# Performance work log

Hardware: AMD Instinct MI355X
Metric: run time of the kernel (lower is better)

## Reference

```python
import jax, jax.numpy as jnp
import numpy as np

N = 100000   # nodes
E = 1600000  # edges
IN_DIM = 256
HID = 128
OUT_DIM = 64
LAYERS = 3
LN_EPS = 1e-5


def _layer_norm(y, g, b):
    mu = jnp.mean(y, axis=-1, keepdims=True)
    var = jnp.mean(jnp.square(y - mu), axis=-1, keepdims=True)
    return (y - mu) * jax.lax.rsqrt(var + LN_EPS) * g + b


def _gcn_conv(x, W, b, src, dst, norm):
    # x: [N, H]; W: [H, H]; src/dst: [E+N] (self-loops appended); norm: [E+N]
    xw = x @ W
    msg = xw[src] * norm[:, None]                       # [E+N, H] gather
    out = jax.ops.segment_sum(msg, dst, num_segments=N)  # scatter-add
    return out + b


def setup_inputs() -> dict:
    key = jax.random.key(0)
    ks = jax.random.split(key, 8)
    x = jax.random.normal(ks[0], (N, IN_DIM), dtype=jnp.float32)
    edge_index = jax.random.randint(ks[1], (2, E), 0, N, dtype=jnp.int32)
    in_W = jax.random.normal(ks[2], (IN_DIM, HID), dtype=jnp.float32) / np.sqrt(IN_DIM).astype(np.float32)
    in_b = jnp.zeros((HID,), jnp.float32)
    conv_W = jax.random.normal(ks[3], (LAYERS, HID, HID), dtype=jnp.float32) / np.sqrt(HID).astype(np.float32)
    conv_b = jnp.zeros((LAYERS, HID), jnp.float32)
    ln_g = jnp.ones((LAYERS, HID), jnp.float32)
    ln_b = jnp.zeros((LAYERS, HID), jnp.float32)
    out_W = jax.random.normal(ks[4], (HID, OUT_DIM), dtype=jnp.float32) / np.sqrt(HID).astype(np.float32)
    out_b = jnp.zeros((OUT_DIM,), jnp.float32)
    return {"x": x, "edge_index": edge_index, "in_W": in_W, "in_b": in_b,
            "conv_W": conv_W, "conv_b": conv_b, "ln_g": ln_g, "ln_b": ln_b,
            "out_W": out_W, "out_b": out_b}


def reference(x, edge_index, in_W, in_b, conv_W, conv_b, ln_g, ln_b, out_W, out_b):
    # add self loops (GCNConv add_self_loops=True, edge_weight=None -> ones)
    loops = jnp.arange(N, dtype=edge_index.dtype)
    src = jnp.concatenate([edge_index[0], loops])
    dst = jnp.concatenate([edge_index[1], loops])
    # symmetric normalization: deg over destination, norm = d^-1/2[src]*d^-1/2[dst]
    deg = jax.ops.segment_sum(jnp.ones_like(src, dtype=jnp.float32), dst, num_segments=N)
    dinv = jnp.where(deg > 0, jax.lax.rsqrt(deg), 0.0)
    norm = dinv[src] * dinv[dst]

    h = x @ in_W + in_b
    for i in range(LAYERS):
        y = _gcn_conv(h, conv_W[i], conv_b[i], src, dst, norm)
        y = _layer_norm(y, ln_g[i], ln_b[i])
        y = jax.nn.relu(y)
        h = h + y  # residual (dropout is identity in eval mode)
    return h @ out_W + out_b
```

## Files before the change

### kernel.cpp

```cpp
#include <hip/hip_runtime.h>
#include <hip/hip_bf16.h>

#define N_NODES 100000
#define E_EDGES 1600000
#define IN_DIM  256
#define HID     128
#define OUT_DIM 64
#define LAYERS  3
#define LN_EPS  1e-5f

typedef __attribute__((ext_vector_type(8)))  short bf16x8;
typedef __attribute__((ext_vector_type(16))) float f32x16;

__device__ inline short f2bf(float f) {
    unsigned u = __float_as_uint(f);
    unsigned r = (u + 0x7fffu + ((u >> 16) & 1u)) >> 16;
    return (short)r;
}
__device__ inline float bflo(unsigned u) { return __uint_as_float(u << 16); }
__device__ inline float bfhi(unsigned u) { return __uint_as_float(u & 0xffff0000u); }


__global__ __launch_bounds__(256) void deg_kernel(const int* __restrict__ dst, int* __restrict__ deg) {
    int e = blockIdx.x * 256 + threadIdx.x;
    if (e < E_EDGES) atomicAdd(&deg[dst[e]], 1);
}

__global__ __launch_bounds__(256) void dinv_kernel(const int* __restrict__ deg, float* __restrict__ dinv) {
    int i = blockIdx.x * 256 + threadIdx.x;
    if (i < N_NODES) dinv[i] = rsqrtf((float)(deg[i] + 1));
}


#define NB_SCAN ((N_NODES + 255) / 256)

__global__ __launch_bounds__(256) void block_sum_kernel(const int* __restrict__ deg,
                                                        int* __restrict__ blockSums) {
    __shared__ int s[256];
    int i = blockIdx.x * 256 + threadIdx.x;
    s[threadIdx.x] = (i < N_NODES) ? deg[i] : 0;
    __syncthreads();
#pragma unroll
    for (int o = 128; o; o >>= 1) {
        if (threadIdx.x < o) s[threadIdx.x] += s[threadIdx.x + o];
        __syncthreads();
    }
    if (threadIdx.x == 0) blockSums[blockIdx.x] = s[0];
}

__global__ __launch_bounds__(512) void scan_blocks_kernel(int* __restrict__ blockSums, int nb) {
    __shared__ int s[512];
    int t = threadIdx.x;
    int orig = (t < nb) ? blockSums[t] : 0;
    s[t] = orig;
    __syncthreads();
#pragma unroll
    for (int o = 1; o < 512; o <<= 1) {
        int v = (t >= o) ? s[t - o] : 0;
        __syncthreads();
        s[t] += v;
        __syncthreads();
    }
    if (t < nb) blockSums[t] = s[t] - orig;
}

__global__ __launch_bounds__(256) void scan_final_kernel(const int* __restrict__ deg,
                                                         const int* __restrict__ blockSums,
                                                         int* __restrict__ offsets,
                                                         int* __restrict__ cursor) {
    __shared__ int s[256];
    int i = blockIdx.x * 256 + threadIdx.x;
    int t = threadIdx.x;
    int v = (i < N_NODES) ? deg[i] : 0;
    s[t] = v;
    __syncthreads();
#pragma unroll
    for (int o = 1; o < 256; o <<= 1) {
        int u = (t >= o) ? s[t - o] : 0;
        __syncthreads();
        s[t] += u;
        __syncthreads();
    }
    if (i < N_NODES) {
        int excl = s[t] - v + blockSums[blockIdx.x];
        offsets[i] = excl;
        cursor[i] = excl;
    }
}

__global__ __launch_bounds__(256) void bin_kernel(const int* __restrict__ src,
                                                  const int* __restrict__ dst,
                                                  const float* __restrict__ dinv,
                                                  int* __restrict__ cursor,
                                                  int2* __restrict__ es) {
    int e = blockIdx.x * 256 + threadIdx.x;
    if (e >= E_EDGES) return;
    int s = src[e], d = dst[e];
    int p = atomicAdd(&cursor[d], 1);
    es[p] = make_int2(s, __float_as_int(dinv[s] * dinv[d]));
}


template<int K, int N>
__global__ __launch_bounds__(256) void wt_kernel(const float* __restrict__ W, short* __restrict__ WT) {
    int idx = blockIdx.x * 256 + threadIdx.x;
    if (idx >= K * N) return;
    int n = idx / K, k = idx % K;
    WT[idx] = f2bf(W[(long)k * N + n]);
}


template<int KT, int N, bool ABF>
__global__ __launch_bounds__(256, 3) void mfma_gemm(const void* __restrict__ Av,
                                                    const short* __restrict__ WT,
                                                    const float* __restrict__ bias,
                                                    float* __restrict__ C,
                                                    short* __restrict__ Cb,
                                                    int M) {
    constexpr int NT = N / 32;
    constexpr int KTS = KT / 16;

    const int tid = threadIdx.x;
    const int wv = tid >> 6;
    const int ln = tid & 63;
    const int l31 = ln & 31;
    const int lh = ln >> 5;
    const int row0 = blockIdx.x * 128 + wv * 32;

    int ar = row0 + l31;
    if (ar > M - 1) ar = M - 1;

    const short* abf = (const short*)Av + (long)ar * KT + lh * 8;
    const float* af32 = (const float*)Av + (long)ar * KT + lh * 8;
    const short* bbase[NT];
#pragma unroll
    for (int nt = 0; nt < NT; nt++)
        bbase[nt] = WT + (long)(nt * 32 + l31) * KT + lh * 8;

    f32x16 acc[NT];
#pragma unroll
    for (int nt = 0; nt < NT; nt++)
#pragma unroll
        for (int r = 0; r < 16; r++) acc[nt][r] = 0.f;

    auto loadA = [&](int ks) -> bf16x8 {
        if (ABF) {
            return *(const bf16x8*)(abf + ks * 16);
        } else {
            float4 f0 = *(const float4*)(af32 + ks * 16);
            float4 f1 = *(const float4*)(af32 + ks * 16 + 4);
            bf16x8 t;
            t[0] = f2bf(f0.x); t[1] = f2bf(f0.y); t[2] = f2bf(f0.z); t[3] = f2bf(f0.w);
            t[4] = f2bf(f1.x); t[5] = f2bf(f1.y); t[6] = f2bf(f1.z); t[7] = f2bf(f1.w);
            return t;
        }
    };

    bf16x8 a_cur, a_nxt;
    bf16x8 b_cur[NT], b_nxt[NT];

    a_cur = loadA(0);
#pragma unroll
    for (int nt = 0; nt < NT; nt++) b_cur[nt] = *(const bf16x8*)(bbase[nt]);

#pragma unroll
    for (int ks = 0; ks < KTS; ks++) {
        if (ks + 1 < KTS) {
            a_nxt = loadA(ks + 1);
#pragma unroll
            for (int nt = 0; nt < NT; nt++)
                b_nxt[nt] = *(const bf16x8*)(bbase[nt] + (ks + 1) * 16);
        }
#pragma unroll
        for (int nt = 0; nt < NT; nt++)
            acc[nt] = __builtin_amdgcn_mfma_f32_32x32x16_bf16(a_cur, b_cur[nt], acc[nt], 0, 0, 0);
        if (ks + 1 < KTS) {
            a_cur = a_nxt;
#pragma unroll
            for (int nt = 0; nt < NT; nt++) b_cur[nt] = b_nxt[nt];
        }
    }

#pragma unroll
    for (int nt = 0; nt < NT; nt++) {
        int col = nt * 32 + l31;
        float bv = bias ? bias[col] : 0.f;
#pragma unroll
        for (int r = 0; r < 16; r++) {
            int row = row0 + (r & 3) + 8 * (r >> 2) + 4 * lh;
            if (row < M) {
                float v = acc[nt][r] + bv;
                if (C)  C[(long)row * N + col] = v;
                if (Cb) Cb[(long)row * N + col] = f2bf(v);
            }
        }
    }
}


__global__ __launch_bounds__(256) void gather_post_kernel(const int* __restrict__ offsets,
                                                          const int* __restrict__ deg,
                                                          const int2* __restrict__ es,
                                                          const float* __restrict__ dinv,
                                                          const short* __restrict__ xwb,
                                                          const float* __restrict__ b,
                                                          const float* __restrict__ g,
                                                          const float* __restrict__ beta,
                                                          float* __restrict__ h,
                                                          short* __restrict__ hb) {
    int wave = threadIdx.x >> 6;
    int lane = threadIdx.x & 63;
    int row = blockIdx.x * 4 + wave;
    if (row >= N_NODES) return;

    const int2* ep = es + offsets[row];
    int dg = deg[row];

    float acc0 = 0.f, acc1 = 0.f;
    int j = 0;
    for (; j + 8 <= dg; j += 8) {
        int2 e0 = ep[j + 0];
        int2 e1 = ep[j + 1];
        int2 e2 = ep[j + 2];
        int2 e3 = ep[j + 3];
        int2 e4 = ep[j + 4];
        int2 e5 = ep[j + 5];
        int2 e6 = ep[j + 6];
        int2 e7 = ep[j + 7];
        unsigned u0 = *(const unsigned*)(&xwb[(long)e0.x * HID + lane * 2]);
        unsigned u1 = *(const unsigned*)(&xwb[(long)e1.x * HID + lane * 2]);
        unsigned u2 = *(const unsigned*)(&xwb[(long)e2.x * HID + lane * 2]);
        unsigned u3 = *(const unsigned*)(&xwb[(long)e3.x * HID + lane * 2]);
        unsigned u4 = *(const unsigned*)(&xwb[(long)e4.x * HID + lane * 2]);
        unsigned u5 = *(const unsigned*)(&xwb[(long)e5.x * HID + lane * 2]);
        unsigned u6 = *(const unsigned*)(&xwb[(long)e6.x * HID + lane * 2]);
        unsigned u7 = *(const unsigned*)(&xwb[(long)e7.x * HID + lane * 2]);
        float w0 = __int_as_float(e0.y), w1 = __int_as_float(e1.y);
        float w2 = __int_as_float(e2.y), w3 = __int_as_float(e3.y);
        float w4 = __int_as_float(e4.y), w5 = __int_as_float(e5.y);
        float w6 = __int_as_float(e6.y), w7 = __int_as_float(e7.y);
        acc0 += bflo(u0) * w0; acc1 += bfhi(u0) * w0;
        acc0 += bflo(u1) * w1; acc1 += bfhi(u1) * w1;
        acc0 += bflo(u2) * w2; acc1 += bfhi(u2) * w2;
        acc0 += bflo(u3) * w3; acc1 += bfhi(u3) * w3;
        acc0 += bflo(u4) * w4; acc1 += bfhi(u4) * w4;
        acc0 += bflo(u5) * w5; acc1 += bfhi(u5) * w5;
        acc0 += bflo(u6) * w6; acc1 += bfhi(u6) * w6;
        acc0 += bflo(u7) * w7; acc1 += bfhi(u7) * w7;
    }
    if (j + 4 <= dg) {
        int2 e0 = ep[j + 0];
        int2 e1 = ep[j + 1];
        int2 e2 = ep[j + 2];
        int2 e3 = ep[j + 3];
        unsigned u0 = *(const unsigned*)(&xwb[(long)e0.x * HID + lane * 2]);
        unsigned u1 = *(const unsigned*)(&xwb[(long)e1.x * HID + lane * 2]);
        unsigned u2 = *(const unsigned*)(&xwb[(long)e2.x * HID + lane * 2]);
        unsigned u3 = *(const unsigned*)(&xwb[(long)e3.x * HID + lane * 2]);
        float w0 = __int_as_float(e0.y), w1 = __int_as_float(e1.y);
        float w2 = __int_as_float(e2.y), w3 = __int_as_float(e3.y);
        acc0 += bflo(u0) * w0; acc1 += bfhi(u0) * w0;
        acc0 += bflo(u1) * w1; acc1 += bfhi(u1) * w1;
        acc0 += bflo(u2) * w2; acc1 += bfhi(u2) * w2;
        acc0 += bflo(u3) * w3; acc1 += bfhi(u3) * w3;
        j += 4;
    }
    for (; j < dg; j++) {
        int2 e0 = ep[j];
        float w0 = __int_as_float(e0.y);
        unsigned u0 = *(const unsigned*)(&xwb[(long)e0.x * HID + lane * 2]);
        acc0 += bflo(u0) * w0; acc1 += bfhi(u0) * w0;
    }

    float di = dinv[row];
    float sw = di * di;
    unsigned ux = *(const unsigned*)(&xwb[(long)row * HID + lane * 2]);
    float2 bv = *reinterpret_cast<const float2*>(&b[lane * 2]);
    float y0 = acc0 + bflo(ux) * sw + bv.x;
    float y1 = acc1 + bfhi(ux) * sw + bv.y;

    float sum = y0 + y1;
#pragma unroll
    for (int o = 32; o; o >>= 1) sum += __shfl_xor(sum, o);
    float mu = sum * (1.0f / HID);

    float d0 = y0 - mu, d1 = y1 - mu;
    float vs = d0 * d0 + d1 * d1;
#pragma unroll
    for (int o = 32; o; o >>= 1) vs += __shfl_xor(vs, o);
    float rstd = rsqrtf(vs * (1.0f / HID) + LN_EPS);

    float2 gv = *reinterpret_cast<const float2*>(&g[lane * 2]);
    float2 bev = *reinterpret_cast<const float2*>(&beta[lane * 2]);
    float r0 = fmaxf(d0 * rstd * gv.x + bev.x, 0.0f);
    float r1 = fmaxf(d1 * rstd * gv.y + bev.y, 0.0f);

    float2* hp = reinterpret_cast<float2*>(&h[(long)row * HID + lane * 2]);
    float2 hv = *hp;
    hv.x += r0;
    hv.y += r1;
    *hp = hv;

    unsigned pk = ((unsigned)(unsigned short)f2bf(hv.y) << 16) |
                  (unsigned)(unsigned short)f2bf(hv.x);
    *reinterpret_cast<unsigned*>(&hb[(long)row * HID + lane * 2]) = pk;
}


extern "C" void kernel_launch(void* const* d_in, const int* in_sizes, int n_in,
                              void* d_out, int out_size, void* d_ws, size_t ws_size,
                              hipStream_t stream) {
    const float* x      = (const float*)d_in[0];
    const int*   eidx   = (const int*)d_in[1];
    const float* in_W   = (const float*)d_in[2];
    const float* in_b   = (const float*)d_in[3];
    const float* conv_W = (const float*)d_in[4];
    const float* conv_b = (const float*)d_in[5];
    const float* ln_g   = (const float*)d_in[6];
    const float* ln_b   = (const float*)d_in[7];
    const float* out_W  = (const float*)d_in[8];
    const float* out_b  = (const float*)d_in[9];

    const int* src = eidx;
    const int* dst = eidx + E_EDGES;

    char* ws = (char*)d_ws;
    size_t off = 0;
    auto alloc = [&](size_t bytes) {
        void* p = ws + off;
        off += (bytes + 1023) & ~(size_t)1023;
        return p;
    };
    int*   deg       = (int*)  alloc((size_t)N_NODES * 4);
    float* dinv      = (float*)alloc((size_t)N_NODES * 4);
    int*   offsets   = (int*)  alloc((size_t)N_NODES * 4);
    int*   cursor    = (int*)  alloc((size_t)N_NODES * 4);
    int*   blockSums = (int*)  alloc((size_t)NB_SCAN * 4);
    int2*  es        = (int2*) alloc((size_t)E_EDGES * 8);
    float* h         = (float*)alloc((size_t)N_NODES * HID * 4);
    short* hb        = (short*)alloc((size_t)N_NODES * HID * 2);
    short* xwb       = (short*)alloc((size_t)N_NODES * HID * 2);
    short* in_WT     = (short*)alloc((size_t)IN_DIM * HID * 2);
    short* conv_WT   = (short*)alloc((size_t)LAYERS * HID * HID * 2);
    short* out_WT    = (short*)alloc((size_t)HID * OUT_DIM * 2);

    hipMemsetAsync(deg, 0, (size_t)N_NODES * 4, stream);
    deg_kernel<<<(E_EDGES + 255) / 256, 256, 0, stream>>>(dst, deg);
    dinv_kernel<<<(N_NODES + 255) / 256, 256, 0, stream>>>(deg, dinv);

    block_sum_kernel<<<NB_SCAN, 256, 0, stream>>>(deg, blockSums);
    scan_blocks_kernel<<<1, 512, 0, stream>>>(blockSums, NB_SCAN);
    scan_final_kernel<<<NB_SCAN, 256, 0, stream>>>(deg, blockSums, offsets, cursor);
    bin_kernel<<<(E_EDGES + 255) / 256, 256, 0, stream>>>(src, dst, dinv, cursor, es);

    wt_kernel<IN_DIM, HID><<<(IN_DIM * HID + 255) / 256, 256, 0, stream>>>(in_W, in_WT);
    for (int l = 0; l < LAYERS; l++)
        wt_kernel<HID, HID><<<(HID * HID + 255) / 256, 256, 0, stream>>>(
            conv_W + (size_t)l * HID * HID, conv_WT + (size_t)l * HID * HID);
    wt_kernel<HID, OUT_DIM><<<(HID * OUT_DIM + 255) / 256, 256, 0, stream>>>(out_W, out_WT);

    const int ggrid = (N_NODES + 127) / 128;

    mfma_gemm<IN_DIM, HID, false><<<ggrid, 256, 0, stream>>>(
        (const void*)x, in_WT, in_b, h, hb, N_NODES);

    for (int l = 0; l < LAYERS; l++) {
        mfma_gemm<HID, HID, true><<<ggrid, 256, 0, stream>>>(
            (const void*)hb, conv_WT + (size_t)l * HID * HID, nullptr, nullptr, xwb, N_NODES);
        gather_post_kernel<<<(N_NODES + 3) / 4, 256, 0, stream>>>(
            offsets, deg, es, dinv, xwb,
            conv_b + l * HID, ln_g + l * HID, ln_b + l * HID, h, hb);
    }

    mfma_gemm<HID, OUT_DIM, true><<<ggrid, 256, 0, stream>>>(
        (const void*)hb, out_WT, out_b, (float*)d_out, nullptr, N_NODES);
}
```

Measured before the change: 735.3 us.

## Factor symmetric GCN norm into GEMM row scale and post-aggregation scale

Splits norm = dinv[src]*dinv[dst] into two factors. The conv GEMM scales each output row by dinv[src], and the gather kernel multiplies the aggregated sum by dinv[dst]. Each CSR edge entry then holds only a 4-byte source index instead of an int2 with a weight, which halves edge-list traffic in the three gather passes and in binning and removes per-edge multiplies. The risk is a small precision change, because the scaled values are rounded to bf16 before aggregation, and the GEMM epilogue loop order is reshuffled.

Result: slower. 752.2 us (+2.3%).

```diff
diff --git a/kernel.cpp b/kernel.cpp
--- a/kernel.cpp
+++ b/kernel.cpp
@@ -90,14 +90,13 @@
 
 __global__ __launch_bounds__(256) void bin_kernel(const int* __restrict__ src,
                                                   const int* __restrict__ dst,
-                                                  const float* __restrict__ dinv,
                                                   int* __restrict__ cursor,
-                                                  int2* __restrict__ es) {
+                                                  int* __restrict__ es) {
     int e = blockIdx.x * 256 + threadIdx.x;
     if (e >= E_EDGES) return;
     int s = src[e], d = dst[e];
     int p = atomicAdd(&cursor[d], 1);
-    es[p] = make_int2(s, __float_as_int(dinv[s] * dinv[d]));
+    es[p] = s;
 }
 
 
@@ -114,6 +113,7 @@
 __global__ __launch_bounds__(256, 3) void mfma_gemm(const void* __restrict__ Av,
                                                     const short* __restrict__ WT,
                                                     const float* __restrict__ bias,
+                                                    const float* __restrict__ scale,
                                                     float* __restrict__ C,
                                                     short* __restrict__ Cb,
                                                     int M) {
@@ -182,17 +182,17 @@
     }
 
 #pragma unroll
-    for (int nt = 0; nt < NT; nt++) {
-        int col = nt * 32 + l31;
-        float bv = bias ? bias[col] : 0.f;
-#pragma unroll
-        for (int r = 0; r < 16; r++) {
-            int row = row0 + (r & 3) + 8 * (r >> 2) + 4 * lh;
-            if (row < M) {
-                float v = acc[nt][r] + bv;
-                if (C)  C[(long)row * N + col] = v;
-                if (Cb) Cb[(long)row * N + col] = f2bf(v);
-            }
+    for (int r = 0; r < 16; r++) {
+        int row = row0 + (r & 3) + 8 * (r >> 2) + 4 * lh;
+        if (row >= M) continue;
+        float sc = scale ? scale[row] : 1.0f;
+#pragma unroll
+        for (int nt = 0; nt < NT; nt++) {
+            int col = nt * 32 + l31;
+            float v = acc[nt][r] + (bias ? bias[col] : 0.0f);
+            v *= sc;
+            if (C)  C[(long)row * N + col] = v;
+            if (Cb) Cb[(long)row * N + col] = f2bf(v);
         }
     }
 }
@@ -200,7 +200,7 @@
 
 __global__ __launch_bounds__(256) void gather_post_kernel(const int* __restrict__ offsets,
                                                           const int* __restrict__ deg,
-                                                          const int2* __restrict__ es,
+                                                          const int* __restrict__ es,
                                                           const float* __restrict__ dinv,
                                                           const short* __restrict__ xwb,
                                                           const float* __restrict__ b,
@@ -213,71 +213,54 @@
     int row = blockIdx.x * 4 + wave;
     if (row >= N_NODES) return;
 
-    const int2* ep = es + offsets[row];
+    const int* ep = es + offsets[row];
     int dg = deg[row];
 
     float acc0 = 0.f, acc1 = 0.f;
     int j = 0;
     for (; j + 8 <= dg; j += 8) {
-        int2 e0 = ep[j + 0];
-        int2 e1 = ep[j + 1];
-        int2 e2 = ep[j + 2];
-        int2 e3 = ep[j + 3];
-        int2 e4 = ep[j + 4];
-        int2 e5 = ep[j + 5];
-        int2 e6 = ep[j + 6];
-        int2 e7 = ep[j + 7];
-        unsigned u0 = *(const unsigned*)(&xwb[(long)e0.x * HID + lane * 2]);
-        unsigned u1 = *(const unsigned*)(&xwb[(long)e1.x * HID + lane * 2]);
-        unsigned u2 = *(const unsigned*)(&xwb[(long)e2.x * HID + lane * 2]);
-        unsigned u3 = *(const unsigned*)(&xwb[(long)e3.x * HID + lane * 2]);
-        unsigned u4 = *(const unsigned*)(&xwb[(long)e4.x * HID + lane * 2]);
-        unsigned u5 = *(const unsigned*)(&xwb[(long)e5.x * HID + lane * 2]);
-        unsigned u6 = *(const unsigned*)(&xwb[(long)e6.x * HID + lane * 2]);
-        unsigned u7 = *(const unsigned*)(&xwb[(long)e7.x * HID + lane * 2]);
-        float w0 = __int_as_float(e0.y), w1 = __int_as_float(e1.y);
-        float w2 = __int_as_float(e2.y), w3 = __int_as_float(e3.y);
-        float w4 = __int_as_float(e4.y), w5 = __int_as_float(e5.y);
-        float w6 = __int_as_float(e6.y), w7 = __int_as_float(e7.y);
-        acc0 += bflo(u0) * w0; acc1 += bfhi(u0) * w0;
-        acc0 += bflo(u1) * w1; acc1 += bfhi(u1) * w1;
-        acc0 += bflo(u2) * w2; acc1 += bfhi(u2) * w2;
-        acc0 += bflo(u3) * w3; acc1 += bfhi(u3) * w3;
-        acc0 += bflo(u4) * w4; acc1 += bfhi(u4) * w4;
-        acc0 += bflo(u5) * w5; acc1 += bfhi(u5) * w5;
-        acc0 += bflo(u6) * w6; acc1 += bfhi(u6) * w6;
-        acc0 += bflo(u7) * w7; acc1 += bfhi(u7) * w7;
+        int s0 = ep[j + 0], s1 = ep[j + 1], s2 = ep[j + 2], s3 = ep[j + 3];
+        int s4 = ep[j + 4], s5 = ep[j + 5], s6 = ep[j + 6], s7 = ep[j + 7];
+        unsigned u0 = *(const unsigned*)(&xwb[(long)s0 * HID + lane * 2]);
+        unsigned u1 = *(const unsigned*)(&xwb[(long)s1 * HID + lane * 2]);
+        unsigned u2 = *(const unsigned*)(&xwb[(long)s2 * HID + lane * 2]);
+        unsigned u3 = *(const unsigned*)(&xwb[(long)s3 * HID + lane * 2]);
+        unsigned u4 = *(const unsigned*)(&xwb[(long)s4 * HID + lane * 2]);
+        unsigned u5 = *(const unsigned*)(&xwb[(long)s5 * HID + lane * 2]);
+        unsigned u6 = *(const unsigned*)(&xwb[(long)s6 * HID + lane * 2]);
+        unsigned u7 = *(const unsigned*)(&xwb[(long)s7 * HID + lane * 2]);
+        acc0 += bflo(u0); acc1 += bfhi(u0);
+        acc0 += bflo(u1); acc1 += bfhi(u1);
+        acc0 += bflo(u2); acc1 += bfhi(u2);
+        acc0 += bflo(u3); acc1 += bfhi(u3);
+        acc0 += bflo(u4); acc1 += bfhi(u4);
+        acc0 += bflo(u5); acc1 += bfhi(u5);
+        acc0 += bflo(u6); acc1 += bfhi(u6);
+        acc0 += bflo(u7); acc1 += bfhi(u7);
     }
     if (j + 4 <= dg) {
-        int2 e0 = ep[j + 0];
-        int2 e1 = ep[j + 1];
-        int2 e2 = ep[j + 2];
-        int2 e3 = ep[j + 3];
-        unsigned u0 = *(const unsigned*)(&xwb[(long)e0.x * HID + lane * 2]);
-        unsigned u1 = *(const unsigned*)(&xwb[(long)e1.x * HID + lane * 2]);
-        unsigned u2 = *(const unsigned*)(&xwb[(long)e2.x * HID + lane * 2]);
-        unsigned u3 = *(const unsigned*)(&xwb[(long)e3.x * HID + lane * 2]);
-        float w0 = __int_as_float(e0.y), w1 = __int_as_float(e1.y);
-        float w2 = __int_as_float(e2.y), w3 = __int_as_float(e3.y);
-        acc0 += bflo(u0) * w0; acc1 += bfhi(u0) * w0;
-        acc0 += bflo(u1) * w1; acc1 += bfhi(u1) * w1;
-        acc0 += bflo(u2) * w2; acc1 += bfhi(u2) * w2;
-        acc0 += bflo(u3) * w3; acc1 += bfhi(u3) * w3;
+        int s0 = ep[j + 0], s1 = ep[j + 1], s2 = ep[j + 2], s3 = ep[j + 3];
+        unsigned u0 = *(const unsigned*)(&xwb[(long)s0 * HID + lane * 2]);
+        unsigned u1 = *(const unsigned*)(&xwb[(long)s1 * HID + lane * 2]);
+        unsigned u2 = *(const unsigned*)(&xwb[(long)s2 * HID + lane * 2]);
+        unsigned u3 = *(const unsigned*)(&xwb[(long)s3 * HID + lane * 2]);
+        acc0 += bflo(u0); acc1 += bfhi(u0);
+        acc0 += bflo(u1); acc1 += bfhi(u1);
+        acc0 += bflo(u2); acc1 += bfhi(u2);
+        acc0 += bflo(u3); acc1 += bfhi(u3);
         j += 4;
     }
     for (; j < dg; j++) {
-        int2 e0 = ep[j];
-        float w0 = __int_as_float(e0.y);
-        unsigned u0 = *(const unsigned*)(&xwb[(long)e0.x * HID + lane * 2]);
-        acc0 += bflo(u0) * w0; acc1 += bfhi(u0) * w0;
+        int s0 = ep[j];
+        unsigned u0 = *(const unsigned*)(&xwb[(long)s0 * HID + lane * 2]);
+        acc0 += bflo(u0); acc1 += bfhi(u0);
     }
 
     float di = dinv[row];
-    float sw = di * di;
     unsigned ux = *(const unsigned*)(&xwb[(long)row * HID + lane * 2]);
     float2 bv = *reinterpret_cast<const float2*>(&b[lane * 2]);
-    float y0 = acc0 + bflo(ux) * sw + bv.x;
-    float y1 = acc1 + bfhi(ux) * sw + bv.y;
+    float y0 = (acc0 + bflo(ux)) * di + bv.x;
+    float y1 = (acc1 + bfhi(ux)) * di + bv.y;
 
     float sum = y0 + y1;
 #pragma unroll
@@ -336,7 +319,7 @@
     int*   offsets   = (int*)  alloc((size_t)N_NODES * 4);
     int*   cursor    = (int*)  alloc((size_t)N_NODES * 4);
     int*   blockSums = (int*)  alloc((size_t)NB_SCAN * 4);
-    int2*  es        = (int2*) alloc((size_t)E_EDGES * 8);
+    int*   es        = (int*)  alloc((size_t)E_EDGES * 4);
     float* h         = (float*)alloc((size_t)N_NODES * HID * 4);
     short* hb        = (short*)alloc((size_t)N_NODES * HID * 2);
     short* xwb       = (short*)alloc((size_t)N_NODES * HID * 2);
@@ -351,7 +334,7 @@
     block_sum_kernel<<<NB_SCAN, 256, 0, stream>>>(deg, blockSums);
     scan_blocks_kernel<<<1, 512, 0, stream>>>(blockSums, NB_SCAN);
     scan_final_kernel<<<NB_SCAN, 256, 0, stream>>>(deg, blockSums, offsets, cursor);
-    bin_kernel<<<(E_EDGES + 255) / 256, 256, 0, stream>>>(src, dst, dinv, cursor, es);
+    bin_kernel<<<(E_EDGES + 255) / 256, 256, 0, stream>>>(src, dst, cursor, es);
 
     wt_kernel<IN_DIM, HID><<<(IN_DIM * HID + 255) / 256, 256, 0, stream>>>(in_W, in_WT);
     for (int l = 0; l < LAYERS; l++)
@@ -362,16 +345,16 @@
     const int ggrid = (N_NODES + 127) / 128;
 
     mfma_gemm<IN_DIM, HID, false><<<ggrid, 256, 0, stream>>>(
-        (const void*)x, in_WT, in_b, h, hb, N_NODES);
+        (const void*)x, in_WT, in_b, nullptr, h, hb, N_NODES);
 
     for (int l = 0; l < LAYERS; l++) {
         mfma_gemm<HID, HID, true><<<ggrid, 256, 0, stream>>>(
-            (const void*)hb, conv_WT + (size_t)l * HID * HID, nullptr, nullptr, xwb, N_NODES);
+            (const void*)hb, conv_WT + (size_t)l * HID * HID, nullptr, dinv, nullptr, xwb, N_NODES);
         gather_post_kernel<<<(N_NODES + 3) / 4, 256, 0, stream>>>(
             offsets, deg, es, dinv, xwb,
             conv_b + l * HID, ln_g + l * HID, ln_b + l * HID, h, hb);
     }
 
     mfma_gemm<HID, OUT_DIM, true><<<ggrid, 256, 0, stream>>>(
-        (const void*)hb, out_WT, out_b, (float*)d_out, nullptr, N_NODES);
-}
+        (const void*)hb, out_WT, out_b, nullptr, (float*)d_out, nullptr, N_NODES);
+}
```
